# Performance work log

Measured on AMD Instinct MI355X. Metric: run time of the kernel, lower is better.

Reference implementation:

```python
import jax, jax.numpy as jnp
import numpy as np

GROUP_SIZES = [16, 16, 16, 16]
K = 2
TEMPERATURE = 1.0
NEG = float(np.finfo(np.float32).min)  # torch.finfo(dtype).min


def setup_inputs() -> dict:
    key = jax.random.key(0)
    k1, k2, k3 = jax.random.split(key, 3)
    B, S, D, E, G = 8, 4096, 1024, 64, len(GROUP_SIZES)
    x = jax.random.normal(k1, (B, S, D), dtype=jnp.float32)
    W_group = jax.random.normal(k2, (G, D), dtype=jnp.float32) * 0.02
    W_expert = jax.random.normal(k3, (E, D), dtype=jnp.float32) * 0.02
    return {"x": x, "W_group": W_group, "W_expert": W_expert}


def reference(x, W_group, W_expert):
    E = W_expert.shape[0]
    # group id of each expert (contiguous ranges) -- static
    expert_group = jnp.asarray(np.repeat(np.arange(len(GROUP_SIZES)), GROUP_SIZES))  # [E]

    # gate logits (no bias), temperature scaling
    expert_logits = jnp.einsum('bsd,ed->bse', x, W_expert) * (1.0 / TEMPERATURE)  # [B,S,E]
    group_logits = jnp.einsum('bsd,gd->bsg', x, W_group)                          # [B,S,G]
    group_probs = jax.nn.softmax(group_logits, axis=-1)
    g_idx = jnp.argmax(group_probs, axis=-1)                                      # [B,S]

    # mask experts outside the selected group's contiguous range
    mask = expert_group[None, None, :] != g_idx[..., None]                        # [B,S,E] bool
    mdt = mask.astype(expert_logits.dtype)
    masked_logits = mdt * NEG + (1.0 - mdt) * expert_logits

    probs_full = jax.nn.softmax(masked_logits, axis=-1)                           # [B,S,E]
    topk_vals, idx = jax.lax.top_k(masked_logits, K)                              # [B,S,K]
    scores = jax.nn.softmax(topk_vals, axis=-1)

    # aux stats (no_grad in original)
    importance = jax.lax.stop_gradient(jnp.mean(probs_full, axis=(0, 1)))         # [E]
    counts = jnp.zeros((E,), probs_full.dtype).at[idx.reshape(-1)].add(1.0)       # [E]
    load = counts / jnp.maximum(jnp.sum(counts), 1.0)
    return (idx, scores, probs_full, importance, load)
```

## Files before the change

kernel.cpp:

```cpp
#include <hip/hip_runtime.h>
#include <math.h>

#define TOKENS   32768
#define DDIM     1024
#define TPB      64
#define NBLOCKS  (TOKENS / TPB)

#define OFF_SCORES 65536
#define OFF_PROBS  131072
#define OFF_IMP    2228224
#define OFF_LOAD   2228288

#define NSLOT 16

typedef __attribute__((ext_vector_type(8))) short  short8;
typedef __attribute__((ext_vector_type(4))) float  f32x4;
typedef __attribute__((ext_vector_type(4))) int    intx4;

__device__ __attribute__((aligned(16))) short wfrag[32 * 5 * 3 * 64 * 8];

__device__ inline unsigned rne_hi(float x) {
  unsigned u = __float_as_uint(x);
  unsigned r = u + 0x7fffu + ((u >> 16) & 1u);
  return r & 0xffff0000u;
}

__device__ inline void split3(const float* xv, short8& f1, short8& f2, short8& f3) {
  int o1[4], o2[4], o3[4];
  #pragma unroll
  for (int p = 0; p < 4; ++p) {
    float x0 = xv[2*p], x1 = xv[2*p+1];
    unsigned h0 = rne_hi(x0), h1 = rne_hi(x1);
    o1[p] = (int)((h0 >> 16) | (h1 & 0xffff0000u));
    float r0 = x0 - __uint_as_float(h0);
    float r1 = x1 - __uint_as_float(h1);
    unsigned g0 = rne_hi(r0), g1 = rne_hi(r1);
    o2[p] = (int)((g0 >> 16) | (g1 & 0xffff0000u));
    float s0 = r0 - __uint_as_float(g0);
    float s1 = r1 - __uint_as_float(g1);
    unsigned w0 = rne_hi(s0), w1 = rne_hi(s1);
    o3[p] = (int)((w0 >> 16) | (w1 & 0xffff0000u));
  }
  intx4 t1 = {o1[0], o1[1], o1[2], o1[3]};
  intx4 t2 = {o2[0], o2[1], o2[2], o2[3]};
  intx4 t3 = {o3[0], o3[1], o3[2], o3[3]};
  f1 = __builtin_bit_cast(short8, t1);
  f2 = __builtin_bit_cast(short8, t2);
  f3 = __builtin_bit_cast(short8, t3);
}

__global__ void prep_kernel(const float* __restrict__ Wg, const float* __restrict__ We) {
  const int nt   = blockIdx.x >> 5;
  const int ks   = blockIdx.x & 31;
  const int lane = threadIdx.x & 63;
  const int row  = nt * 16 + (lane & 15);
  const int k0   = ks * 32 + (lane >> 4) * 8;
  float xv[8];
  #pragma unroll
  for (int j = 0; j < 8; ++j) {
    float v = 0.f;
    if (row < 64)      v = We[(size_t)row * DDIM + k0 + j];
    else if (row < 68) v = Wg[(size_t)(row - 64) * DDIM + k0 + j];
    xv[j] = v;
  }
  short8 f1, f2, f3;
  split3(xv, f1, f2, f3);
  short8* dst = (short8*)wfrag + (((size_t)ks * 5 + nt) * 3) * 64 + lane;
  dst[0]   = f1;
  dst[64]  = f2;
  dst[128] = f3;
}

__global__ __launch_bounds__(128)
__attribute__((amdgpu_waves_per_eu(1, 1)))
void router_kernel(const float* __restrict__ x,
                   float* __restrict__ out,
                   float* __restrict__ ws) {
  __shared__ __attribute__((aligned(16))) float el[TPB * 88];
  __shared__ int cnt[64];
  const int tid    = threadIdx.x;
  const int lane   = tid & 63;
  const int khalf  = tid >> 6;
  const int quad   = lane >> 4;
  const int m      = lane & 15;
  const int tokblk = blockIdx.x * TPB;

  if (tid < 64) cnt[tid] = 0;

  const float* apb = x + (size_t)(tokblk + m) * DDIM + khalf * 512 + quad * 8;

  f32x4 ahi[4][5], alo[4][5];
  #pragma unroll
  for (int mt = 0; mt < 4; ++mt)
    #pragma unroll
    for (int nt = 0; nt < 5; ++nt) { ahi[mt][nt] = 0.f; alo[mt][nt] = 0.f; }

  float4 cur[8], nxt[8];
  #pragma unroll
  for (int mt = 0; mt < 4; ++mt) {
    const float* p = apb + (size_t)(mt * 16) * DDIM;
    cur[mt * 2]     = *(const float4*)(p);
    cur[mt * 2 + 1] = *(const float4*)(p + 4);
  }

  for (int ks = 0; ks < 16; ++ks) {
    const short8* bp = (const short8*)wfrag + ((size_t)(khalf * 16 + ks) * 15) * 64 + lane;
    short8 fb[5][3];
    #pragma unroll
    for (int nt = 0; nt < 5; ++nt) {
      fb[nt][0] = bp[nt * 192];
      fb[nt][1] = bp[nt * 192 + 64];
      fb[nt][2] = bp[nt * 192 + 128];
    }
    const int kpf = (ks + 1 < 16) ? (ks + 1) : 15;
    #pragma unroll
    for (int mt = 0; mt < 4; ++mt) {
      const float* p = apb + (size_t)(mt * 16) * DDIM + kpf * 32;
      nxt[mt * 2]     = *(const float4*)(p);
      nxt[mt * 2 + 1] = *(const float4*)(p + 4);
    }
    short8 fa[4][3];
    #pragma unroll
    for (int mt = 0; mt < 4; ++mt) {
      float av[8] = {cur[mt*2].x, cur[mt*2].y, cur[mt*2].z, cur[mt*2].w,
                     cur[mt*2+1].x, cur[mt*2+1].y, cur[mt*2+1].z, cur[mt*2+1].w};
      split3(av, fa[mt][0], fa[mt][1], fa[mt][2]);
    }
    #pragma unroll
    for (int nt = 0; nt < 5; ++nt)
      #pragma unroll
      for (int mt = 0; mt < 4; ++mt) {
        ahi[mt][nt] = __builtin_amdgcn_mfma_f32_16x16x32_bf16(fa[mt][0], fb[nt][0], ahi[mt][nt], 0, 0, 0);
        f32x4 c = alo[mt][nt];
        c = __builtin_amdgcn_mfma_f32_16x16x32_bf16(fa[mt][0], fb[nt][1], c, 0, 0, 0);
        c = __builtin_amdgcn_mfma_f32_16x16x32_bf16(fa[mt][1], fb[nt][0], c, 0, 0, 0);
        c = __builtin_amdgcn_mfma_f32_16x16x32_bf16(fa[mt][1], fb[nt][1], c, 0, 0, 0);
        c = __builtin_amdgcn_mfma_f32_16x16x32_bf16(fa[mt][0], fb[nt][2], c, 0, 0, 0);
        c = __builtin_amdgcn_mfma_f32_16x16x32_bf16(fa[mt][2], fb[nt][0], c, 0, 0, 0);
        c = __builtin_amdgcn_mfma_f32_16x16x32_bf16(fa[mt][1], fb[nt][2], c, 0, 0, 0);
        c = __builtin_amdgcn_mfma_f32_16x16x32_bf16(fa[mt][2], fb[nt][1], c, 0, 0, 0);
        alo[mt][nt] = c;
      }
    #pragma unroll
    for (int i = 0; i < 8; ++i) cur[i] = nxt[i];
  }

  if (khalf == 1) {
    #pragma unroll
    for (int mt = 0; mt < 4; ++mt)
      #pragma unroll
      for (int nt = 0; nt < 5; ++nt)
        #pragma unroll
        for (int r = 0; r < 4; ++r)
          el[(mt * 16 + quad * 4 + r) * 88 + nt * 16 + m] = ahi[mt][nt][r] + alo[mt][nt][r];
  }
  __syncthreads();
  if (khalf == 0) {
    #pragma unroll
    for (int mt = 0; mt < 4; ++mt)
      #pragma unroll
      for (int nt = 0; nt < 5; ++nt)
        #pragma unroll
        for (int r = 0; r < 4; ++r) {
          const int idx = (mt * 16 + quad * 4 + r) * 88 + nt * 16 + m;
          el[idx] += ahi[mt][nt][r] + alo[mt][nt][r];
        }
  }
  __syncthreads();

  if (tid < TPB) {
    const int t = tid;
    float* row = el + t * 88;
    const float g0 = row[64], g1 = row[65], g2 = row[66], g3 = row[67];
    int g = 0; float gb = g0;
    if (g1 > gb) { g = 1; gb = g1; }
    if (g2 > gb) { g = 2; gb = g2; }
    if (g3 > gb) { g = 3; gb = g3; }
    const int base = g << 4;
    float l[16];
    #pragma unroll
    for (int e = 0; e < 16; ++e) l[e] = row[base + e];
    int i1 = 0; float v1 = l[0];
    #pragma unroll
    for (int e = 1; e < 16; ++e) if (l[e] > v1) { i1 = e; v1 = l[e]; }
    int i2 = -1; float v2 = 0.f;
    #pragma unroll
    for (int e = 0; e < 16; ++e) {
      if (e == i1) continue;
      if (i2 < 0 || l[e] > v2) { i2 = e; v2 = l[e]; }
    }
    float pr[16]; float s = 0.f;
    #pragma unroll
    for (int e = 0; e < 16; ++e) { pr[e] = expf(l[e] - v1); s += pr[e]; }
    const float inv = 1.f / s;
    #pragma unroll
    for (int c = 0; c < 64; ++c) row[c] = 0.f;
    #pragma unroll
    for (int e = 0; e < 16; ++e) row[base + e] = pr[e] * inv;
    const size_t T = (size_t)tokblk + t;
    out[2*T]     = (float)(base + i1);
    out[2*T + 1] = (float)(base + i2);
    const float e2 = expf(v2 - v1);
    const float si = 1.f / (1.f + e2);
    out[OFF_SCORES + 2*T]     = si;
    out[OFF_SCORES + 2*T + 1] = e2 * si;
    atomicAdd(&cnt[base + i1], 1);
    atomicAdd(&cnt[base + i2], 1);
  }
  __syncthreads();

  for (int i = tid; i < TPB * 64; i += 128) {
    const int t = i >> 6, c = i & 63;
    out[OFF_PROBS + (((size_t)(tokblk + t)) << 6) + c] = el[t * 88 + c];
  }
  if (tid < 64) {
    const int e = tid;
    float s = 0.f;
    #pragma unroll 4
    for (int t = 0; t < TPB; ++t) s += el[t * 88 + e];
    const int slot = (blockIdx.x & (NSLOT - 1)) * 128;
    atomicAdd(&ws[slot + e], s);
    atomicAdd(&ws[slot + 64 + e], (float)cnt[e]);
  }
}

__global__ void finalize_kernel(const float* __restrict__ ws, float* __restrict__ out) {
  const int e = threadIdx.x;
  if (e < 64) {
    float imp = 0.f, cf = 0.f;
    #pragma unroll
    for (int s = 0; s < NSLOT; ++s) {
      imp += ws[s * 128 + e];
      cf  += ws[s * 128 + 64 + e];
    }
    out[OFF_IMP  + e] = imp * (1.0f / 32768.0f);
    out[OFF_LOAD + e] = cf  * (1.0f / 65536.0f);
  }
}

extern "C" void kernel_launch(void* const* d_in, const int* in_sizes, int n_in,
                              void* d_out, int out_size, void* d_ws, size_t ws_size,
                              hipStream_t stream) {
  (void)in_sizes; (void)n_in; (void)out_size; (void)ws_size;
  const float* x  = (const float*)d_in[0];
  const float* Wg = (const float*)d_in[1];
  const float* We = (const float*)d_in[2];
  float* out = (float*)d_out;
  float* ws  = (float*)d_ws;
  hipMemsetAsync(d_ws, 0, NSLOT * 128 * sizeof(float), stream);
  hipLaunchKernelGGL(prep_kernel, dim3(160), dim3(64), 0, stream, Wg, We);
  hipLaunchKernelGGL(router_kernel, dim3(NBLOCKS), dim3(128), 0, stream, x, out, ws);
  hipLaunchKernelGGL(finalize_kernel, dim3(1), dim3(64), 0, stream, ws, out);
}
```

Before: 210.4 us.

## Deepen x prefetch to two stages and fold aux reduction into router atomics

The register prefetch of x tiles now runs two k-steps ahead instead of one, so more global-load latency is hidden behind MFMA work. The memset and finalize kernel are removed: prep_kernel zeroes the importance/load outputs and each router block atomically adds pre-scaled sums straight into the output. This cuts two launches but sends all 512 blocks' atomics to one 64-entry location instead of 16 slots, adding contention and changing float summation order. The extra prefetch buffer also raises register pressure in a kernel already pinned to one wave per EU.

```diff
diff --git a/kernel.cpp b/kernel.cpp
--- a/kernel.cpp
+++ b/kernel.cpp
@@ -10,8 +10,6 @@
 #define OFF_PROBS  131072
 #define OFF_IMP    2228224
 #define OFF_LOAD   2228288
-
-#define NSLOT 16
 
 typedef __attribute__((ext_vector_type(8))) short  short8;
 typedef __attribute__((ext_vector_type(4))) float  f32x4;
@@ -49,10 +47,15 @@
   f3 = __builtin_bit_cast(short8, t3);
 }
 
-__global__ void prep_kernel(const float* __restrict__ Wg, const float* __restrict__ We) {
+__global__ void prep_kernel(const float* __restrict__ Wg, const float* __restrict__ We,
+                            float* __restrict__ out) {
   const int nt   = blockIdx.x >> 5;
   const int ks   = blockIdx.x & 31;
   const int lane = threadIdx.x & 63;
+  if (blockIdx.x == 0) {
+    out[OFF_IMP  + lane] = 0.f;
+    out[OFF_LOAD + lane] = 0.f;
+  }
   const int row  = nt * 16 + (lane & 15);
   const int k0   = ks * 32 + (lane >> 4) * 8;
   float xv[8];
@@ -74,8 +77,7 @@
 __global__ __launch_bounds__(128)
 __attribute__((amdgpu_waves_per_eu(1, 1)))
 void router_kernel(const float* __restrict__ x,
-                   float* __restrict__ out,
-                   float* __restrict__ ws) {
+                   float* __restrict__ out) {
   __shared__ __attribute__((aligned(16))) float el[TPB * 88];
   __shared__ int cnt[64];
   const int tid    = threadIdx.x;
@@ -95,12 +97,14 @@
     #pragma unroll
     for (int nt = 0; nt < 5; ++nt) { ahi[mt][nt] = 0.f; alo[mt][nt] = 0.f; }
 
-  float4 cur[8], nxt[8];
+  float4 cur[8], nx1[8], nx2[8];
   #pragma unroll
   for (int mt = 0; mt < 4; ++mt) {
     const float* p = apb + (size_t)(mt * 16) * DDIM;
     cur[mt * 2]     = *(const float4*)(p);
     cur[mt * 2 + 1] = *(const float4*)(p + 4);
+    nx1[mt * 2]     = *(const float4*)(p + 32);
+    nx1[mt * 2 + 1] = *(const float4*)(p + 36);
   }
 
   for (int ks = 0; ks < 16; ++ks) {
@@ -112,12 +116,12 @@
       fb[nt][1] = bp[nt * 192 + 64];
       fb[nt][2] = bp[nt * 192 + 128];
     }
-    const int kpf = (ks + 1 < 16) ? (ks + 1) : 15;
+    const int kpf = (ks + 2 < 16) ? (ks + 2) : 15;
     #pragma unroll
     for (int mt = 0; mt < 4; ++mt) {
       const float* p = apb + (size_t)(mt * 16) * DDIM + kpf * 32;
-      nxt[mt * 2]     = *(const float4*)(p);
-      nxt[mt * 2 + 1] = *(const float4*)(p + 4);
+      nx2[mt * 2]     = *(const float4*)(p);
+      nx2[mt * 2 + 1] = *(const float4*)(p + 4);
     }
     short8 fa[4][3];
     #pragma unroll
@@ -142,7 +146,7 @@
         alo[mt][nt] = c;
       }
     #pragma unroll
-    for (int i = 0; i < 8; ++i) cur[i] = nxt[i];
+    for (int i = 0; i < 8; ++i) { cur[i] = nx1[i]; nx1[i] = nx2[i]; }
   }
 
   if (khalf == 1) {
@@ -218,37 +222,19 @@
     float s = 0.f;
     #pragma unroll 4
     for (int t = 0; t < TPB; ++t) s += el[t * 88 + e];
-    const int slot = (blockIdx.x & (NSLOT - 1)) * 128;
-    atomicAdd(&ws[slot + e], s);
-    atomicAdd(&ws[slot + 64 + e], (float)cnt[e]);
-  }
-}
-
-__global__ void finalize_kernel(const float* __restrict__ ws, float* __restrict__ out) {
-  const int e = threadIdx.x;
-  if (e < 64) {
-    float imp = 0.f, cf = 0.f;
-    #pragma unroll
-    for (int s = 0; s < NSLOT; ++s) {
-      imp += ws[s * 128 + e];
-      cf  += ws[s * 128 + 64 + e];
-    }
-    out[OFF_IMP  + e] = imp * (1.0f / 32768.0f);
-    out[OFF_LOAD + e] = cf  * (1.0f / 65536.0f);
+    atomicAdd(&out[OFF_IMP  + e], s * (1.0f / 32768.0f));
+    atomicAdd(&out[OFF_LOAD + e], (float)cnt[e] * (1.0f / 65536.0f));
   }
 }
 
 extern "C" void kernel_launch(void* const* d_in, const int* in_sizes, int n_in,
                               void* d_out, int out_size, void* d_ws, size_t ws_size,
                               hipStream_t stream) {
-  (void)in_sizes; (void)n_in; (void)out_size; (void)ws_size;
+  (void)in_sizes; (void)n_in; (void)out_size; (void)d_ws; (void)ws_size;
   const float* x  = (const float*)d_in[0];
   const float* Wg = (const float*)d_in[1];
   const float* We = (const float*)d_in[2];
   float* out = (float*)d_out;
-  float* ws  = (float*)d_ws;
-  hipMemsetAsync(d_ws, 0, NSLOT * 128 * sizeof(float), stream);
-  hipLaunchKernelGGL(prep_kernel, dim3(160), dim3(64), 0, stream, Wg, We);
-  hipLaunchKernelGGL(router_kernel, dim3(NBLOCKS), dim3(128), 0, stream, x, out, ws);
-  hipLaunchKernelGGL(finalize_kernel, dim3(1), dim3(64), 0, stream, ws, out);
-}
+  hipLaunchKernelGGL(prep_kernel, dim3(160), dim3(64), 0, stream, Wg, We, out);
+  hipLaunchKernelGGL(router_kernel, dim3(NBLOCKS), dim3(128), 0, stream, x, out);
+}
```

Result: slower. 244.3 us (+16.1%).
